# Kernel optimization log

Hardware: AMD Instinct MI355X
Metric: run time of the kernel (lower is better)

Reference implementation:

```python
import jax, jax.numpy as jnp
import numpy as np

B, D, C = 1024, 128, 100000
EPS = 1e-12  # torch F.normalize eps


def setup_inputs() -> dict:
    key = jax.random.key(0)
    k1, k2, k3 = jax.random.split(key, 3)
    # scale so ||x||^2 ~ 1, keeping exp(-dist) in a representable range
    xs = jax.random.normal(k1, (B, D), dtype=jnp.float32) / np.sqrt(D)
    ys = jax.random.randint(k2, (B,), 0, C, dtype=jnp.int64)
    # xavier_uniform init of Embedding(C, D): U(-a, a), a = sqrt(6/(C+D))
    a = np.sqrt(6.0 / (C + D))
    proxies = jax.random.uniform(k3, (C, D), dtype=jnp.float32, minval=-a, maxval=a)
    return {"xs": xs, "ys": ys, "proxies": proxies}


def reference(xs, ys, proxies):
    # L2-normalize every proxy (original normalizes pos proxy over dim=0 of a 1-D
    # vector and neg proxies over dim=1 -- both are per-proxy L2 normalization).
    norm = jnp.linalg.norm(proxies, axis=1, keepdims=True)
    P = proxies / jnp.maximum(norm, EPS)                      # [C, D], unit rows
    x_sq = jnp.sum(xs * xs, axis=1, keepdims=True)            # [B, 1]
    d = x_sq + 1.0 - 2.0 * (xs @ P.T)                         # [B, C]
    e = jnp.exp(-d)                                           # [B, C]
    pos = jnp.take_along_axis(e, ys[:, None], axis=1)[:, 0]   # exp(-d[b, y_b])
    neg_sum = jnp.sum(e, axis=1) - pos                        # denominator excludes the positive
    return jnp.mean(-jnp.log(pos / neg_sum))
```

## Files before the change

kernel.cpp:

```cpp
#include <hip/hip_runtime.h>
#include <hip/hip_fp16.h>

#define B_N 1024
#define D_K 128
#define C_N 100000
#define CCHUNK 80
#define NCC 1250
#define BSPLIT 2
#define NBLK_MAIN (NCC * BSPLIT)
#define NREP 8
#define EPSN 1e-12f
#define XSCL 2.8853900817779268f

typedef _Float16 half8 __attribute__((ext_vector_type(8)));
typedef float floatx4 __attribute__((ext_vector_type(4)));

union U16 { uint4 u; half8 h; };

#if __has_builtin(__builtin_amdgcn_exp2f)
__device__ __forceinline__ float exp2_hw(float x) { return __builtin_amdgcn_exp2f(x); }
#else
__device__ __forceinline__ float exp2_hw(float x) {
    float r; asm("v_exp_f32 %0, %1" : "=v"(r) : "v"(x)); return r;
}
#endif

__device__ __forceinline__ unsigned int pack2h(float a, float b) {
    union { _Float16 h[2]; unsigned int u; } p;
    p.h[0] = (_Float16)a; p.h[1] = (_Float16)b;
    return p.u;
}

__global__ __launch_bounds__(256) void prep_kernel(
    const float* __restrict__ xs, const int* __restrict__ ys,
    const float* __restrict__ proxies,
    unsigned int* __restrict__ xfrag, float* __restrict__ w,
    float* __restrict__ posd, float* __restrict__ negsumR)
{
    int tid  = threadIdx.x;
    int gid  = blockIdx.x * 256 + tid;
    if (gid < B_N * NREP) negsumR[gid] = 0.0f;

    int wave = tid >> 6, lane = tid & 63;
    int b = blockIdx.x * 4 + wave;

    const float2 xv = ((const float2*)(xs + (size_t)b * D_K))[lane];
    float ss = xv.x * xv.x + xv.y * xv.y;
    #pragma unroll
    for (int m = 1; m < 64; m <<= 1) ss += __shfl_xor(ss, m, 64);
    float xsq = ss;

    {
        int f  = lane >> 4;
        int m4 = (lane >> 2) & 3;
        int j  = lane & 3;
        int idx = ((((b >> 4) * 4 + f) * 64) + ((b & 15) | (m4 << 4))) * 4 + j;
        xfrag[idx] = pack2h(XSCL * xv.x, XSCL * xv.y);
    }

    int y = ys[b];
    const float2 pv = ((const float2*)(proxies + (size_t)y * D_K))[lane];
    float dt = xv.x * pv.x + xv.y * pv.y;
    float pp = pv.x * pv.x + pv.y * pv.y;
    #pragma unroll
    for (int m = 1; m < 64; m <<= 1) {
        dt += __shfl_xor(dt, m, 64);
        pp += __shfl_xor(pp, m, 64);
    }
    if (lane == 0) {
        w[b] = __expf(-xsq - 1.0f);
        float nrm = fmaxf(sqrtf(pp), EPSN);
        posd[b] = xsq + 1.0f - 2.0f * (dt / nrm);
    }
}

__device__ __forceinline__ void stage_row(
    uint4* __restrict__ ldsP,
    float4 v0, float4 v1, float4 v2, float4 v3, int r, int L)
{
    float ss = v0.x*v0.x + v0.y*v0.y + v0.z*v0.z + v0.w*v0.w
             + v1.x*v1.x + v1.y*v1.y + v1.z*v1.z + v1.w*v1.w
             + v2.x*v2.x + v2.y*v2.y + v2.z*v2.z + v2.w*v2.w
             + v3.x*v3.x + v3.y*v3.y + v3.z*v3.z + v3.w*v3.w;
    ss += __shfl_xor(ss, 1, 64);
    ss += __shfl_xor(ss, 2, 64);
    ss += __shfl_xor(ss, 4, 64);
    float sc = 1.0f / fmaxf(sqrtf(ss), EPSN);

    union { _Float16 h[8]; uint4 u; } pa, pb;
    pa.h[0]=(_Float16)(v0.x*sc); pa.h[1]=(_Float16)(v0.y*sc);
    pa.h[2]=(_Float16)(v0.z*sc); pa.h[3]=(_Float16)(v0.w*sc);
    pa.h[4]=(_Float16)(v1.x*sc); pa.h[5]=(_Float16)(v1.y*sc);
    pa.h[6]=(_Float16)(v1.z*sc); pa.h[7]=(_Float16)(v1.w*sc);
    pb.h[0]=(_Float16)(v2.x*sc); pb.h[1]=(_Float16)(v2.y*sc);
    pb.h[2]=(_Float16)(v2.z*sc); pb.h[3]=(_Float16)(v2.w*sc);
    pb.h[4]=(_Float16)(v3.x*sc); pb.h[5]=(_Float16)(v3.y*sc);
    pb.h[6]=(_Float16)(v3.z*sc); pb.h[7]=(_Float16)(v3.w*sc);

    int cb = r >> 4, rc = r & 15;
    int f  = L >> 1;
    int mA = (L * 2) & 3;
    int mB = (L * 2 + 1) & 3;
    ldsP[(cb * 4 + f) * 64 + (rc | (mA << 4))] = pa.u;
    ldsP[(cb * 4 + f) * 64 + (rc | (mB << 4))] = pb.u;
}

__global__ __launch_bounds__(256, 4) void main_kernel(
    const float* __restrict__ proxies,
    const uint4* __restrict__ xfrag,
    float* __restrict__ negsumR)
{
    __shared__ uint4 ldsP[CCHUNK * 8];

    int tid = threadIdx.x;
    int bx  = blockIdx.x;
    int cc  = bx >> 1;
    int bs  = bx & 1;
    int c0  = cc * CCHUNK;

    {
        int L  = tid & 7;
        int rb = tid >> 3;
        const float* base = proxies + (size_t)c0 * D_K + L * 16;
        const float4* s0 = (const float4*)(base + (size_t)rb * D_K);
        const float4* s1 = (const float4*)(base + (size_t)(rb + 32) * D_K);
        float4 A0 = s0[0], A1 = s0[1], A2 = s0[2], A3 = s0[3];
        float4 B0 = s1[0], B1 = s1[1], B2 = s1[2], B3 = s1[3];
        float4 C0, C1, C2, C3;
        if (rb < 16) {
            const float4* s2 = (const float4*)(base + (size_t)(rb + 64) * D_K);
            C0 = s2[0]; C1 = s2[1]; C2 = s2[2]; C3 = s2[3];
        }
        stage_row(ldsP, A0, A1, A2, A3, rb,      L);
        stage_row(ldsP, B0, B1, B2, B3, rb + 32, L);
        if (rb < 16)
            stage_row(ldsP, C0, C1, C2, C3, rb + 64, L);
    }
    __syncthreads();

    int wave  = tid >> 6, lane = tid & 63;
    int b0    = bs * 512 + wave * 128;
    int t0    = b0 >> 4;
    float* nsr = negsumR + (size_t)(bx & (NREP - 1)) * B_N;

    #pragma unroll 1
    for (int bg = 0; bg < 4; ++bg) {
        uint4 xf[2][4];
        #pragma unroll
        for (int bt = 0; bt < 2; ++bt)
            #pragma unroll
            for (int f = 0; f < 4; ++f)
                xf[bt][f] = xfrag[((t0 + bg * 2 + bt) * 4 + f) * 64 + lane];

        float sv[2] = {0.f, 0.f};

        #pragma unroll 1
        for (int cb = 0; cb < CCHUNK / 16; ++cb) {
            uint4 a[4];
            #pragma unroll
            for (int f = 0; f < 4; ++f)
                a[f] = ldsP[(cb * 4 + f) * 64 + lane];

            #pragma unroll
            for (int bt = 0; bt < 2; ++bt) {
                floatx4 acc = {0.f, 0.f, 0.f, 0.f};
                #pragma unroll
                for (int f = 0; f < 4; ++f) {
                    U16 ua, ub;
                    ua.u = a[f];
                    ub.u = xf[bt][f];
                    acc = __builtin_amdgcn_mfma_f32_16x16x32_f16(ua.h, ub.h, acc, 0, 0, 0);
                }
                sv[bt] += exp2_hw(acc[0]) + exp2_hw(acc[1])
                        + exp2_hw(acc[2]) + exp2_hw(acc[3]);
            }
        }

        #pragma unroll
        for (int bt = 0; bt < 2; ++bt) {
            float v = sv[bt];
            v += __shfl_xor(v, 16, 64);
            v += __shfl_xor(v, 32, 64);
            if (lane < 16)
                atomicAdd(&nsr[b0 + bg * 32 + bt * 16 + lane], v);
        }
    }
}

__global__ __launch_bounds__(1024) void final_kernel(
    const float* __restrict__ negsumR, const float* __restrict__ w,
    const float* __restrict__ posd, float* __restrict__ out)
{
    __shared__ float red[1024];
    int t = threadIdx.x;
    float ns = 0.0f;
    #pragma unroll
    for (int r = 0; r < NREP; ++r) ns += negsumR[r * B_N + t];
    float pd = posd[t];
    red[t] = logf(ns * w[t] - __expf(-pd)) + pd;
    __syncthreads();
    #pragma unroll
    for (int s = 512; s > 0; s >>= 1) {
        if (t < s) red[t] += red[t + s];
        __syncthreads();
    }
    if (t == 0) out[0] = red[0] * (1.0f / 1024.0f);
}

extern "C" void kernel_launch(void* const* d_in, const int* in_sizes, int n_in,
                              void* d_out, int out_size, void* d_ws, size_t ws_size,
                              hipStream_t stream)
{
    const float* xs      = (const float*)d_in[0];
    const int*   ys      = (const int*)d_in[1];
    const float* proxies = (const float*)d_in[2];

    char* ws = (char*)d_ws;
    unsigned int* xfrag = (unsigned int*)ws;
    float* w       = (float*)(ws + 262144);
    float* posd    = (float*)(ws + 262144 + 4096);
    float* negsumR = (float*)(ws + 262144 + 8192);

    prep_kernel<<<256, 256, 0, stream>>>(xs, ys, proxies, xfrag, w, posd, negsumR);
    main_kernel<<<NBLK_MAIN, 256, 0, stream>>>(proxies, (const uint4*)ws, negsumR);
    final_kernel<<<1, 1024, 0, stream>>>(negsumR, w, posd, (float*)d_out);
}
```

Before: 115.6 us.

## Make main kernel persistent with prefetched proxy chunks and fused final reduction

The main kernel becomes persistent: each block keeps one quarter of the batch fragments in registers and strides over five proxy chunks. The next chunk's global loads are issued while the current chunk's MFMA/exp work runs, and staging uses double-buffered LDS. The separate final kernel is removed; the last block to finish, found through an atomic done-counter, computes the loss. This removes a kernel launch, cuts repeated xfrag reloads and hides load latency, at the cost of higher register pressure (occupancy hint lowered to 3) and a serialized tail in the last block.

```diff
diff --git a/kernel.cpp b/kernel.cpp
--- a/kernel.cpp
+++ b/kernel.cpp
@@ -6,8 +6,11 @@
 #define C_N 100000
 #define CCHUNK 80
 #define NCC 1250
-#define BSPLIT 2
-#define NBLK_MAIN (NCC * BSPLIT)
+#define SSTRIDE 250
+#define NQ 4
+#define NPART (NQ * SSTRIDE)
+#define GRID_MAIN 1024
+#define NCHUNKS_PER_BLK 5
 #define NREP 8
 #define EPSN 1e-12f
 #define XSCL 2.8853900817779268f
@@ -35,11 +38,13 @@
     const float* __restrict__ xs, const int* __restrict__ ys,
     const float* __restrict__ proxies,
     unsigned int* __restrict__ xfrag, float* __restrict__ w,
-    float* __restrict__ posd, float* __restrict__ negsumR)
+    float* __restrict__ posd, float* __restrict__ negsumR,
+    unsigned int* __restrict__ donecnt)
 {
     int tid  = threadIdx.x;
     int gid  = blockIdx.x * 256 + tid;
     if (gid < B_N * NREP) negsumR[gid] = 0.0f;
+    if (gid == B_N * NREP) *donecnt = 0u;
 
     int wave = tid >> 6, lane = tid & 63;
     int b = blockIdx.x * 4 + wave;
@@ -75,7 +80,7 @@
 }
 
 __device__ __forceinline__ void stage_row(
-    uint4* __restrict__ ldsP,
+    uint4* __restrict__ lp,
     float4 v0, float4 v1, float4 v2, float4 v3, int r, int L)
 {
     float ss = v0.x*v0.x + v0.y*v0.y + v0.z*v0.z + v0.w*v0.w
@@ -101,68 +106,92 @@
     int f  = L >> 1;
     int mA = (L * 2) & 3;
     int mB = (L * 2 + 1) & 3;
-    ldsP[(cb * 4 + f) * 64 + (rc | (mA << 4))] = pa.u;
-    ldsP[(cb * 4 + f) * 64 + (rc | (mB << 4))] = pb.u;
-}
-
-__global__ __launch_bounds__(256, 4) void main_kernel(
+    lp[(cb * 4 + f) * 64 + (rc | (mA << 4))] = pa.u;
+    lp[(cb * 4 + f) * 64 + (rc | (mB << 4))] = pb.u;
+}
+
+__global__ __launch_bounds__(256, 3) void main_kernel(
     const float* __restrict__ proxies,
     const uint4* __restrict__ xfrag,
-    float* __restrict__ negsumR)
-{
-    __shared__ uint4 ldsP[CCHUNK * 8];
+    const float* __restrict__ w, const float* __restrict__ posd,
+    float* __restrict__ negsumR, unsigned int* __restrict__ donecnt,
+    float* __restrict__ out)
+{
+    __shared__ uint4 ldsP[2][CCHUNK * 8];
+    __shared__ int lastBlk;
+    __shared__ float redf[4];
 
     int tid = threadIdx.x;
     int bx  = blockIdx.x;
-    int cc  = bx >> 1;
-    int bs  = bx & 1;
-    int c0  = cc * CCHUNK;
+
+    int s8  = bx & 7;
+    int g   = bx >> 3;
+    int q   = g & 3;
+    int shi = g >> 2;
+    int s   = shi * 8 + s8;
+    if (s >= SSTRIDE) return;
+
+    int wave = tid >> 6, lane = tid & 63;
+
+    int t0 = q * 16 + wave * 4;
+    uint4 xf[4][4];
+    #pragma unroll
+    for (int bt = 0; bt < 4; ++bt)
+        #pragma unroll
+        for (int f = 0; f < 4; ++f)
+            xf[bt][f] = xfrag[((t0 + bt) * 4 + f) * 64 + lane];
+
+    float sv[4] = {0.f, 0.f, 0.f, 0.f};
+
+    int L  = tid & 7;
+    int rb = tid >> 3;
+    float4 A0, A1, A2, A3, B0, B1, B2, B3, C0, C1, C2, C3;
 
     {
-        int L  = tid & 7;
-        int rb = tid >> 3;
-        const float* base = proxies + (size_t)c0 * D_K + L * 16;
+        const float* base = proxies + (size_t)(s * CCHUNK) * D_K + L * 16;
         const float4* s0 = (const float4*)(base + (size_t)rb * D_K);
         const float4* s1 = (const float4*)(base + (size_t)(rb + 32) * D_K);
-        float4 A0 = s0[0], A1 = s0[1], A2 = s0[2], A3 = s0[3];
-        float4 B0 = s1[0], B1 = s1[1], B2 = s1[2], B3 = s1[3];
-        float4 C0, C1, C2, C3;
+        A0 = s0[0]; A1 = s0[1]; A2 = s0[2]; A3 = s0[3];
+        B0 = s1[0]; B1 = s1[1]; B2 = s1[2]; B3 = s1[3];
         if (rb < 16) {
             const float4* s2 = (const float4*)(base + (size_t)(rb + 64) * D_K);
             C0 = s2[0]; C1 = s2[1]; C2 = s2[2]; C3 = s2[3];
         }
-        stage_row(ldsP, A0, A1, A2, A3, rb,      L);
-        stage_row(ldsP, B0, B1, B2, B3, rb + 32, L);
+    }
+
+    int buf = 0;
+    #pragma unroll 1
+    for (int it = 0; it < NCHUNKS_PER_BLK; ++it) {
+        uint4* lp = &ldsP[buf][0];
+
+        stage_row(lp, A0, A1, A2, A3, rb,      L);
+        stage_row(lp, B0, B1, B2, B3, rb + 32, L);
         if (rb < 16)
-            stage_row(ldsP, C0, C1, C2, C3, rb + 64, L);
-    }
-    __syncthreads();
-
-    int wave  = tid >> 6, lane = tid & 63;
-    int b0    = bs * 512 + wave * 128;
-    int t0    = b0 >> 4;
-    float* nsr = negsumR + (size_t)(bx & (NREP - 1)) * B_N;
-
-    #pragma unroll 1
-    for (int bg = 0; bg < 4; ++bg) {
-        uint4 xf[2][4];
-        #pragma unroll
-        for (int bt = 0; bt < 2; ++bt)
-            #pragma unroll
-            for (int f = 0; f < 4; ++f)
-                xf[bt][f] = xfrag[((t0 + bg * 2 + bt) * 4 + f) * 64 + lane];
-
-        float sv[2] = {0.f, 0.f};
+            stage_row(lp, C0, C1, C2, C3, rb + 64, L);
+        __syncthreads();
+
+        if (it < NCHUNKS_PER_BLK - 1) {
+            const float* base = proxies
+                + (size_t)((s + (it + 1) * SSTRIDE) * CCHUNK) * D_K + L * 16;
+            const float4* s0 = (const float4*)(base + (size_t)rb * D_K);
+            const float4* s1 = (const float4*)(base + (size_t)(rb + 32) * D_K);
+            A0 = s0[0]; A1 = s0[1]; A2 = s0[2]; A3 = s0[3];
+            B0 = s1[0]; B1 = s1[1]; B2 = s1[2]; B3 = s1[3];
+            if (rb < 16) {
+                const float4* s2 = (const float4*)(base + (size_t)(rb + 64) * D_K);
+                C0 = s2[0]; C1 = s2[1]; C2 = s2[2]; C3 = s2[3];
+            }
+        }
 
         #pragma unroll 1
         for (int cb = 0; cb < CCHUNK / 16; ++cb) {
             uint4 a[4];
             #pragma unroll
             for (int f = 0; f < 4; ++f)
-                a[f] = ldsP[(cb * 4 + f) * 64 + lane];
+                a[f] = lp[(cb * 4 + f) * 64 + lane];
 
             #pragma unroll
-            for (int bt = 0; bt < 2; ++bt) {
+            for (int bt = 0; bt < 4; ++bt) {
                 floatx4 acc = {0.f, 0.f, 0.f, 0.f};
                 #pragma unroll
                 for (int f = 0; f < 4; ++f) {
@@ -175,36 +204,46 @@
                         + exp2_hw(acc[2]) + exp2_hw(acc[3]);
             }
         }
-
+        buf ^= 1;
+    }
+
+    float* nsr = negsumR + (size_t)(bx & (NREP - 1)) * B_N;
+    #pragma unroll
+    for (int bt = 0; bt < 4; ++bt) {
+        float v = sv[bt];
+        v += __shfl_xor(v, 16, 64);
+        v += __shfl_xor(v, 32, 64);
+        if (lane < 16)
+            atomicAdd(&nsr[q * 256 + wave * 64 + bt * 16 + lane], v);
+    }
+
+    __threadfence();
+    __syncthreads();
+    if (tid == 0) {
+        unsigned int old = atomicAdd(donecnt, 1u);
+        lastBlk = (old == NPART - 1) ? 1 : 0;
+    }
+    __syncthreads();
+    if (lastBlk) {
+        float part = 0.0f;
         #pragma unroll
-        for (int bt = 0; bt < 2; ++bt) {
-            float v = sv[bt];
-            v += __shfl_xor(v, 16, 64);
-            v += __shfl_xor(v, 32, 64);
-            if (lane < 16)
-                atomicAdd(&nsr[b0 + bg * 32 + bt * 16 + lane], v);
-        }
-    }
-}
-
-__global__ __launch_bounds__(1024) void final_kernel(
-    const float* __restrict__ negsumR, const float* __restrict__ w,
-    const float* __restrict__ posd, float* __restrict__ out)
-{
-    __shared__ float red[1024];
-    int t = threadIdx.x;
-    float ns = 0.0f;
-    #pragma unroll
-    for (int r = 0; r < NREP; ++r) ns += negsumR[r * B_N + t];
-    float pd = posd[t];
-    red[t] = logf(ns * w[t] - __expf(-pd)) + pd;
-    __syncthreads();
-    #pragma unroll
-    for (int s = 512; s > 0; s >>= 1) {
-        if (t < s) red[t] += red[t + s];
+        for (int i = 0; i < 4; ++i) {
+            int b = tid + i * 256;
+            float ns = 0.0f;
+            #pragma unroll
+            for (int r = 0; r < NREP; ++r)
+                ns += __hip_atomic_load(&negsumR[r * B_N + b],
+                                        __ATOMIC_RELAXED, __HIP_MEMORY_SCOPE_AGENT);
+            float pd = posd[b];
+            part += logf(ns * w[b] - __expf(-pd)) + pd;
+        }
+        #pragma unroll
+        for (int m = 1; m < 64; m <<= 1) part += __shfl_xor(part, m, 64);
+        if (lane == 0) redf[wave] = part;
         __syncthreads();
-    }
-    if (t == 0) out[0] = red[0] * (1.0f / 1024.0f);
+        if (tid == 0)
+            out[0] = (redf[0] + redf[1] + redf[2] + redf[3]) * (1.0f / 1024.0f);
+    }
 }
 
 extern "C" void kernel_launch(void* const* d_in, const int* in_sizes, int n_in,
@@ -216,12 +255,14 @@
     const float* proxies = (const float*)d_in[2];
 
     char* ws = (char*)d_ws;
-    unsigned int* xfrag = (unsigned int*)ws;
-    float* w       = (float*)(ws + 262144);
-    float* posd    = (float*)(ws + 262144 + 4096);
-    float* negsumR = (float*)(ws + 262144 + 8192);
-
-    prep_kernel<<<256, 256, 0, stream>>>(xs, ys, proxies, xfrag, w, posd, negsumR);
-    main_kernel<<<NBLK_MAIN, 256, 0, stream>>>(proxies, (const uint4*)ws, negsumR);
-    final_kernel<<<1, 1024, 0, stream>>>(negsumR, w, posd, (float*)d_out);
-}
+    unsigned int* xfrag   = (unsigned int*)ws;
+    float* w              = (float*)(ws + 262144);
+    float* posd           = (float*)(ws + 262144 + 4096);
+    float* negsumR        = (float*)(ws + 262144 + 8192);
+    unsigned int* donecnt = (unsigned int*)(ws + 262144 + 8192 + 32768);
+
+    prep_kernel<<<256, 256, 0, stream>>>(xs, ys, proxies, xfrag, w, posd,
+                                         negsumR, donecnt);
+    main_kernel<<<GRID_MAIN, 256, 0, stream>>>(proxies, (const uint4*)ws, w, posd,
+                                               negsumR, donecnt, (float*)d_out);
+}
```

Result: slower. 185.9 us (+60.8%).
